# Performance work log

Measured on AMD Instinct MI355X. Metric: run time of the kernel, lower is better.

The kernel has to match this reference:

```python
import jax, jax.numpy as jnp
import numpy as np

B, IN_DIM, HID, DIM, M = 4096, 256, 200, 512, 256


def setup_inputs() -> dict:
    key = jax.random.key(0)
    ks = jax.random.split(key, 9)
    x = jax.random.normal(ks[0], (B, IN_DIM), dtype=jnp.float32)
    # per-sample polytope RHS; strictly positive so y=0 is always feasible
    b = jax.random.uniform(ks[1], (B, M), dtype=jnp.float32) + 1.0
    W1 = jax.random.normal(ks[2], (IN_DIM, HID), dtype=jnp.float32) / np.sqrt(IN_DIM)
    b1 = jnp.zeros((HID,), dtype=jnp.float32)
    W2 = jax.random.normal(ks[3], (HID, HID), dtype=jnp.float32) / np.sqrt(HID)
    b2 = jnp.zeros((HID,), dtype=jnp.float32)
    W3 = jax.random.normal(ks[4], (HID, DIM), dtype=jnp.float32) / np.sqrt(HID)
    b3 = jnp.zeros((DIM,), dtype=jnp.float32)
    # constraint matrix A: polytope {y : A y <= b}
    A = jax.random.normal(ks[5], (M, DIM), dtype=jnp.float32) / np.sqrt(DIM)
    return {"x": x, "b": b, "W1": W1, "b1": b1, "W2": W2, "b2": b2,
            "W3": W3, "b3": b3, "A": A, "step": 0, "n_iter": 100}


def _mlp(x, W1, b1, W2, b2, W3, b3):
    h = jax.nn.relu(x @ W1 + b1)
    h = jax.nn.relu(h @ W2 + b2)
    return h @ W3 + b3  # [B, DIM]


def _project(y0, b, A, n_iter):
    """Euclidean projection of y0 onto {y : A y <= b} via dual projected gradient.
    y(lam) = y0 - A^T lam;  lam <- relu(lam + t (A y(lam) - b))."""
    t = 1.0 / jnp.sum(A * A)  # 1/||A||_F^2 <= 1/sigma_max(A)^2 -> convergent step

    def body(lam, _):
        y = y0 - lam @ A                      # [B, DIM]
        lam = jax.nn.relu(lam + t * (y @ A.T - b))  # [B, M]
        return lam, None

    lam0 = jnp.zeros_like(b)
    lam, _ = jax.lax.scan(body, lam0, None, length=n_iter)
    return y0 - lam @ A


def reference(x, b, W1, b1, W2, b2, W3, b3, A, step, n_iter):
    y0 = _mlp(x, W1, b1, W2, b2, W3, b3)
    # optax.linear_schedule(0.0, 0.0, 2000, 300) is identically zero
    alpha = jnp.float32(0.0)
    y = _project(y0, b, A, n_iter)
    return (1.0 - alpha) * y + alpha * y0
```

## Files before the change

kernel.cpp:

```cpp
#include <hip/hip_runtime.h>
#include <hip/hip_bf16.h>
#include <stdint.h>


typedef __attribute__((ext_vector_type(8))) short bf16x8;
typedef __attribute__((ext_vector_type(4))) float f32x4;
typedef __attribute__((ext_vector_type(4))) unsigned short u16x4;

__device__ __forceinline__ unsigned short f2b(float f) {
  union { float f; uint32_t u; } v; v.f = f;
  uint32_t r = (v.u + 0x7FFFu + ((v.u >> 16) & 1u)) >> 16;
  return (unsigned short)r;
}
__device__ __forceinline__ float b2f(unsigned short h) {
  union { uint32_t u; float f; } v; v.u = ((uint32_t)h) << 16;
  return v.f;
}
__device__ __forceinline__ unsigned int pk2(float a, float b) {
  __hip_bfloat162 h = __float22bfloat162_rn(make_float2(a, b));
  unsigned int u; __builtin_memcpy(&u, &h, 4); return u;
}
__device__ __forceinline__ float ldf(const void* p, int idx, int f32f) {
  return f32f ? ((const float*)p)[idx] : b2f(((const unsigned short*)p)[idx]);
}
__device__ __forceinline__ f32x4 mfma16(bf16x8 a, bf16x8 b, f32x4 c) {
  return __builtin_amdgcn_mfma_f32_16x16x32_bf16(a, b, c, 0, 0, 0);
}
__device__ __forceinline__ bf16x8 ld8(const void* p, int idx, int f32f) {
  bf16x8 r;
  if (f32f) {
    float4 a0 = *(const float4*)((const float*)p + idx);
    float4 a1 = *(const float4*)((const float*)p + idx + 4);
    r[0]=(short)f2b(a0.x); r[1]=(short)f2b(a0.y); r[2]=(short)f2b(a0.z); r[3]=(short)f2b(a0.w);
    r[4]=(short)f2b(a1.x); r[5]=(short)f2b(a1.y); r[6]=(short)f2b(a1.z); r[7]=(short)f2b(a1.w);
  } else {
    r = *(const bf16x8*)((const unsigned short*)p + idx);
  }
  return r;
}
__device__ __forceinline__ int sniff(const void* p) {
  unsigned short h = ((const unsigned short*)p)[threadIdx.x & 63];
  unsigned e = (h >> 7) & 0xFFu;
  return (__ballot(e >= 132u) != 0ull) ? 1 : 0;
}

__device__ __forceinline__ void swiz_one(const void* __restrict__ src,
                                         unsigned short* __restrict__ dst, int e,
                                         int Ksrc, int Nsrc, int ld, bool trans,
                                         int NCT, int f32f) {
  const int j = e & 7, lane = (e >> 3) & 63, rest = e >> 9;
  const int nt = rest % NCT, kk = rest / NCT;
  const int k = kk * 32 + ((lane >> 4) << 3) + j;
  const int n = nt * 16 + (lane & 15);
  unsigned short v = 0;
  if (k < Ksrc && n < Nsrc)
    v = f2b(ldf(src, trans ? n * ld + k : k * ld + n, f32f));
  dst[e] = v;
}

__global__ __launch_bounds__(256) void prep_kernel(
    const void* __restrict__ W1, const void* __restrict__ W2,
    const void* __restrict__ W3, const void* __restrict__ Am,
    unsigned short* __restrict__ Gsw, float* __restrict__ slot,
    unsigned short* __restrict__ W1sw, unsigned short* __restrict__ W2sw,
    unsigned short* __restrict__ W3sw, unsigned short* __restrict__ ATsw,
    unsigned short* __restrict__ Asw) {
  const int f32f = sniff(Am);
  const int tid = threadIdx.x;
  if (blockIdx.x < 256) {
    if (tid >= 64) return;
    const int lane = tid, r16 = lane & 15, q = lane >> 4;
    const int ti = blockIdx.x >> 4, tj = blockIdx.x & 15;
    const int rowA = (16 * ti + r16) * 512;
    const int rowB = (16 * tj + r16) * 512;
    f32x4 acc = {0.f, 0.f, 0.f, 0.f};
    #pragma unroll
    for (int kk = 0; kk < 16; ++kk) {
      const int col = 32 * kk + 8 * q;
      bf16x8 afr = ld8(Am, rowA + col, f32f);
      bf16x8 bfr = ld8(Am, rowB + col, f32f);
      acc = mfma16(afr, bfr, acc);
    }
    #pragma unroll
    for (int rg = 0; rg < 4; ++rg) {
      const int mrow = 16 * ti + 4 * q + rg;
      const int kk2 = mrow >> 5, q2 = (mrow >> 3) & 3, j = mrow & 7;
      Gsw[((kk2 * 16 + tj) * 64 + (q2 * 16 + r16)) * 8 + j] = f2b(acc[rg]);
    }
    if (ti == tj) {
      float d = ((r16 >> 2) == q) ? acc[r16 & 3] : 0.0f;
      #pragma unroll
      for (int off = 32; off >= 1; off >>= 1) d += __shfl_xor(d, off, 64);
      if (lane == 0) slot[ti] = d;
    }
    return;
  }
  int idx = (blockIdx.x - 256) * 256 + tid;
  if (idx < 53248)  { swiz_one(W1, W1sw, idx, 256, 200, 200, false, 13, f32f); return; }
  idx -= 53248;
  if (idx < 46592)  { swiz_one(W2, W2sw, idx, 200, 200, 200, false, 13, f32f); return; }
  idx -= 46592;
  if (idx < 114688) { swiz_one(W3, W3sw, idx, 200, 512, 512, false, 32, f32f); return; }
  idx -= 114688;
  if (idx < 131072) { swiz_one(Am, ATsw, idx, 512, 256, 512, true, 16, f32f); return; }
  idx -= 131072;
  swiz_one(Am, Asw, idx, 256, 512, 512, false, 32, f32f);
}

__global__ __launch_bounds__(512, 2) void mega_kernel(
    const void* __restrict__ x,
    const void* __restrict__ bmat,
    const void* __restrict__ b1,
    const void* __restrict__ b2,
    const void* __restrict__ b3,
    const float* __restrict__ slot,
    const unsigned short* __restrict__ Gsw,
    const unsigned short* __restrict__ W1sw,
    const unsigned short* __restrict__ W2sw,
    const unsigned short* __restrict__ W3sw,
    const unsigned short* __restrict__ ATsw,
    const unsigned short* __restrict__ Asw,
    float* __restrict__ out)
{
  __shared__ __attribute__((aligned(16))) unsigned short xbuf[16 * 264];
  __shared__ __attribute__((aligned(16))) unsigned short hbuf[16 * 232];
  __shared__ __attribute__((aligned(16))) unsigned short ybuf[16 * 520];
  __shared__ __attribute__((aligned(16))) unsigned short lbuf[2][16 * 264];
  __shared__ __attribute__((aligned(16))) float yf32[16 * 516];

  const int tid = threadIdx.x;
  const int lane = tid & 63;
  const int w = tid >> 6;
  const int r16 = lane & 15;
  const int q = lane >> 4;
  const int rowbase = blockIdx.x << 4;
  const int f32f = sniff(x);

  {
    const int rr = tid >> 5;
    const int c8 = (tid & 31) << 3;
    if (f32f) {
      const float4* sp = (const float4*)((const float*)x + (rowbase + rr) * 256 + c8);
      float4 v0 = sp[0], v1 = sp[1];
      u16x4 p0 = {f2b(v0.x), f2b(v0.y), f2b(v0.z), f2b(v0.w)};
      u16x4 p1 = {f2b(v1.x), f2b(v1.y), f2b(v1.z), f2b(v1.w)};
      *(u16x4*)&xbuf[rr * 264 + c8]     = p0;
      *(u16x4*)&xbuf[rr * 264 + c8 + 4] = p1;
    } else {
      *(bf16x8*)&xbuf[rr * 264 + c8] =
          *(const bf16x8*)((const unsigned short*)x + (rowbase + rr) * 256 + c8);
    }
    if (tid < 256) hbuf[(tid >> 4) * 232 + 208 + (tid & 15)] = 0;
  }
  __syncthreads();
  float tr = 0.0f;
  #pragma unroll
  for (int i = 0; i < 16; ++i) tr += slot[i];
  const float t = 1.0f / tr;

  f32x4 a1[2];
  #pragma unroll
  for (int i = 0; i < 2; ++i) a1[i] = (f32x4){0.f, 0.f, 0.f, 0.f};
  #pragma unroll
  for (int kk = 0; kk < 8; ++kk) {
    bf16x8 bx = *(const bf16x8*)&xbuf[r16 * 264 + 32 * kk + 8 * q];
    #pragma unroll
    for (int i = 0; i < 2; ++i) {
      const int nt = w + 8 * i;
      if (nt < 13) {
        bf16x8 af = *(const bf16x8*)(W1sw + ((kk * 13 + nt) * 64 + lane) * 8);
        a1[i] = mfma16(af, bx, a1[i]);
      }
    }
  }
  #pragma unroll
  for (int i = 0; i < 2; ++i) {
    const int nt = w + 8 * i;
    if (nt < 13) {
      u16x4 pk;
      #pragma unroll
      for (int rg = 0; rg < 4; ++rg) {
        const int n = 16 * nt + 4 * q + rg;
        const float bias = (n < 200) ? ldf(b1, n, f32f) : 0.0f;
        pk[rg] = f2b(fmaxf(a1[i][rg] + bias, 0.0f));
      }
      *(u16x4*)&hbuf[r16 * 232 + 16 * nt + 4 * q] = pk;
    }
  }
  __syncthreads();

  f32x4 a2[2];
  #pragma unroll
  for (int i = 0; i < 2; ++i) a2[i] = (f32x4){0.f, 0.f, 0.f, 0.f};
  #pragma unroll
  for (int kk = 0; kk < 7; ++kk) {
    bf16x8 bh = *(const bf16x8*)&hbuf[r16 * 232 + 32 * kk + 8 * q];
    #pragma unroll
    for (int i = 0; i < 2; ++i) {
      const int nt = w + 8 * i;
      if (nt < 13) {
        bf16x8 af = *(const bf16x8*)(W2sw + ((kk * 13 + nt) * 64 + lane) * 8);
        a2[i] = mfma16(af, bh, a2[i]);
      }
    }
  }
  __syncthreads();
  #pragma unroll
  for (int i = 0; i < 2; ++i) {
    const int nt = w + 8 * i;
    if (nt < 13) {
      u16x4 pk;
      #pragma unroll
      for (int rg = 0; rg < 4; ++rg) {
        const int n = 16 * nt + 4 * q + rg;
        const float bias = (n < 200) ? ldf(b2, n, f32f) : 0.0f;
        pk[rg] = f2b(fmaxf(a2[i][rg] + bias, 0.0f));
      }
      *(u16x4*)&hbuf[r16 * 232 + 16 * nt + 4 * q] = pk;
    }
  }
  __syncthreads();

  {
    f32x4 y0a[4];
    #pragma unroll
    for (int i = 0; i < 4; ++i) y0a[i] = (f32x4){0.f, 0.f, 0.f, 0.f};
    #pragma unroll
    for (int kk = 0; kk < 7; ++kk) {
      bf16x8 bh = *(const bf16x8*)&hbuf[r16 * 232 + 32 * kk + 8 * q];
      #pragma unroll
      for (int i = 0; i < 4; ++i) {
        const int nt = 4 * w + i;
        bf16x8 af = *(const bf16x8*)(W3sw + ((kk * 32 + nt) * 64 + lane) * 8);
        y0a[i] = mfma16(af, bh, y0a[i]);
      }
    }
    #pragma unroll
    for (int i = 0; i < 4; ++i) {
      const int nt = 4 * w + i;
      u16x4 pk;
      #pragma unroll
      for (int rg = 0; rg < 4; ++rg) {
        y0a[i][rg] += ldf(b3, 16 * nt + 4 * q + rg, f32f);
        pk[rg] = f2b(y0a[i][rg]);
      }
      *(u16x4*)&ybuf[r16 * 520 + 16 * nt + 4 * q] = pk;
      float4 sf = {y0a[i][0], y0a[i][1], y0a[i][2], y0a[i][3]};
      *(float4*)&yf32[r16 * 516 + 16 * nt + 4 * q] = sf;
    }
  }
  __syncthreads();

  f32x4 tc[4], base[4];
  if (w < 4) {
    f32x4 cacc[4];
    #pragma unroll
    for (int i = 0; i < 4; ++i) {
      const int mt = w + 4 * i;
      if (f32f) {
        float4 bb = *(const float4*)((const float*)bmat + (rowbase + r16) * 256 + 16 * mt + 4 * q);
        cacc[i] = (f32x4){-bb.x, -bb.y, -bb.z, -bb.w};
      } else {
        u16x4 bb = *(const u16x4*)((const unsigned short*)bmat + (rowbase + r16) * 256 + 16 * mt + 4 * q);
        #pragma unroll
        for (int rg = 0; rg < 4; ++rg) cacc[i][rg] = -b2f(bb[rg]);
      }
    }
    #pragma unroll
    for (int kk = 0; kk < 16; ++kk) {
      bf16x8 by = *(const bf16x8*)&ybuf[r16 * 520 + 32 * kk + 8 * q];
      #pragma unroll
      for (int i = 0; i < 4; ++i) {
        bf16x8 af = *(const bf16x8*)(ATsw + ((kk * 16 + w + 4 * i) * 64 + lane) * 8);
        cacc[i] = mfma16(af, by, cacc[i]);
      }
    }
    #pragma unroll
    for (int i = 0; i < 4; ++i) {
      #pragma unroll
      for (int rg = 0; rg < 4; ++rg) {
        tc[i][rg] = t * cacc[i][rg];
        base[i][rg] = fmaxf(tc[i][rg], 0.0f) + tc[i][rg];
      }
      const unsigned int lo = pk2(fmaxf(tc[i][0], 0.f), fmaxf(tc[i][1], 0.f));
      const unsigned int hi = pk2(fmaxf(tc[i][2], 0.f), fmaxf(tc[i][3], 0.f));
      *(uint2*)&lbuf[0][r16 * 264 + 16 * (w + 4 * i) + 4 * q] = make_uint2(lo, hi);
    }
  }

  bf16x8 gA0, gA1, gA2, gA3, gA4, gA5, gA6, gA7;
  bf16x8 gB0, gB1, gB2, gB3, gB4, gB5, gB6, gB7;
  bf16x8 gC0, gC1, gC2, gC3, gC4, gC5, gC6, gC7;
  bf16x8 gD0, gD1, gD2, gD3, gD4, gD5, gD6, gD7;
  if (w < 4) {
    #define GLD(j, i) (*(const bf16x8*)(Gsw + (((j) * 16 + w + 4 * (i)) * 64 + lane) * 8))
    gA0 = GLD(0,0); gA1 = GLD(1,0); gA2 = GLD(2,0); gA3 = GLD(3,0);
    gA4 = GLD(4,0); gA5 = GLD(5,0); gA6 = GLD(6,0); gA7 = GLD(7,0);
    gB0 = GLD(0,1); gB1 = GLD(1,1); gB2 = GLD(2,1); gB3 = GLD(3,1);
    gB4 = GLD(4,1); gB5 = GLD(5,1); gB6 = GLD(6,1); gB7 = GLD(7,1);
    gC0 = GLD(0,2); gC1 = GLD(1,2); gC2 = GLD(2,2); gC3 = GLD(3,2);
    gC4 = GLD(4,2); gC5 = GLD(5,2); gC6 = GLD(6,2); gC7 = GLD(7,2);
    gD0 = GLD(0,3); gD1 = GLD(1,3); gD2 = GLD(2,3); gD3 = GLD(3,3);
    gD4 = GLD(4,3); gD5 = GLD(5,3); gD6 = GLD(6,3); gD7 = GLD(7,3);
    #undef GLD
    asm volatile("" : "+v"(gA0), "+v"(gA1), "+v"(gA2), "+v"(gA3),
                      "+v"(gA4), "+v"(gA5), "+v"(gA6), "+v"(gA7),
                      "+v"(gB0), "+v"(gB1), "+v"(gB2), "+v"(gB3),
                      "+v"(gB4), "+v"(gB5), "+v"(gB6), "+v"(gB7));
    asm volatile("" : "+v"(gC0), "+v"(gC1), "+v"(gC2), "+v"(gC3),
                      "+v"(gC4), "+v"(gC5), "+v"(gC6), "+v"(gC7),
                      "+v"(gD0), "+v"(gD1), "+v"(gD2), "+v"(gD3),
                      "+v"(gD4), "+v"(gD5), "+v"(gD6), "+v"(gD7));
  }
  __syncthreads();

  #define PGD_J(j, blv) \
    acc0 = mfma16(gA##j, blv, acc0); acc1 = mfma16(gB##j, blv, acc1); \
    acc2 = mfma16(gC##j, blv, acc2); acc3 = mfma16(gD##j, blv, acc3);
  int cur = 0;
  for (int it = 0; it < 99; ++it) {
    if (w < 4) {
      const unsigned short* lb = &lbuf[cur][r16 * 264 + 8 * q];
      const bf16x8 bl0 = *(const bf16x8*)(lb);
      const bf16x8 bl1 = *(const bf16x8*)(lb + 32);
      const bf16x8 bl2 = *(const bf16x8*)(lb + 64);
      const bf16x8 bl3 = *(const bf16x8*)(lb + 96);
      const bf16x8 bl4 = *(const bf16x8*)(lb + 128);
      const bf16x8 bl5 = *(const bf16x8*)(lb + 160);
      const bf16x8 bl6 = *(const bf16x8*)(lb + 192);
      const bf16x8 bl7 = *(const bf16x8*)(lb + 224);
      f32x4 acc0 = {0.f, 0.f, 0.f, 0.f}, acc1 = {0.f, 0.f, 0.f, 0.f};
      f32x4 acc2 = {0.f, 0.f, 0.f, 0.f}, acc3 = {0.f, 0.f, 0.f, 0.f};
      PGD_J(0, bl0)  PGD_J(1, bl1)  PGD_J(2, bl2)  PGD_J(3, bl3)
      PGD_J(4, bl4)  PGD_J(5, bl5)  PGD_J(6, bl6)  PGD_J(7, bl7)
      const unsigned int sx = (it == 98) ? 0x80008000u : 0u;
      const int nxt = cur ^ 1;
      {
        f32x4 v;
        #pragma unroll
        for (int rg = 0; rg < 4; ++rg)
          v[rg] = fmaxf(fmaf(-t, acc0[rg], base[0][rg]), 0.0f);
        *(uint2*)&lbuf[nxt][r16 * 264 + 16 * w + 4 * q] =
            make_uint2(pk2(v[0], v[1]) ^ sx, pk2(v[2], v[3]) ^ sx);
        #pragma unroll
        for (int rg = 0; rg < 4; ++rg) base[0][rg] = v[rg] + tc[0][rg];
      }
      {
        f32x4 v;
        #pragma unroll
        for (int rg = 0; rg < 4; ++rg)
          v[rg] = fmaxf(fmaf(-t, acc1[rg], base[1][rg]), 0.0f);
        *(uint2*)&lbuf[nxt][r16 * 264 + 16 * (w + 4) + 4 * q] =
            make_uint2(pk2(v[0], v[1]) ^ sx, pk2(v[2], v[3]) ^ sx);
        #pragma unroll
        for (int rg = 0; rg < 4; ++rg) base[1][rg] = v[rg] + tc[1][rg];
      }
      {
        f32x4 v;
        #pragma unroll
        for (int rg = 0; rg < 4; ++rg)
          v[rg] = fmaxf(fmaf(-t, acc2[rg], base[2][rg]), 0.0f);
        *(uint2*)&lbuf[nxt][r16 * 264 + 16 * (w + 8) + 4 * q] =
            make_uint2(pk2(v[0], v[1]) ^ sx, pk2(v[2], v[3]) ^ sx);
        #pragma unroll
        for (int rg = 0; rg < 4; ++rg) base[2][rg] = v[rg] + tc[2][rg];
      }
      {
        f32x4 v;
        #pragma unroll
        for (int rg = 0; rg < 4; ++rg)
          v[rg] = fmaxf(fmaf(-t, acc3[rg], base[3][rg]), 0.0f);
        *(uint2*)&lbuf[nxt][r16 * 264 + 16 * (w + 12) + 4 * q] =
            make_uint2(pk2(v[0], v[1]) ^ sx, pk2(v[2], v[3]) ^ sx);
        #pragma unroll
        for (int rg = 0; rg < 4; ++rg) base[3][rg] = v[rg] + tc[3][rg];
      }
    }
    __syncthreads();
    cur ^= 1;
  }
  #undef PGD_J

  f32x4 yo[4];
  #pragma unroll
  for (int i = 0; i < 4; ++i) {
    float4 v = *(const float4*)&yf32[r16 * 516 + 16 * (4 * w + i) + 4 * q];
    yo[i] = (f32x4){v.x, v.y, v.z, v.w};
  }
  #pragma unroll
  for (int kk = 0; kk < 8; ++kk) {
    bf16x8 bl = *(const bf16x8*)&lbuf[cur][r16 * 264 + 32 * kk + 8 * q];
    #pragma unroll
    for (int i = 0; i < 4; ++i) {
      bf16x8 af = *(const bf16x8*)(Asw + ((kk * 32 + 4 * w + i) * 64 + lane) * 8);
      yo[i] = mfma16(af, bl, yo[i]);
    }
  }
  #pragma unroll
  for (int i = 0; i < 4; ++i) {
    const int nt = 4 * w + i;
    float4 st = {yo[i][0], yo[i][1], yo[i][2], yo[i][3]};
    *(float4*)(out + (size_t)(rowbase + r16) * 512 + 16 * nt + 4 * q) = st;
  }
}

extern "C" void kernel_launch(void* const* d_in, const int* in_sizes, int n_in,
                              void* d_out, int out_size, void* d_ws, size_t ws_size,
                              hipStream_t stream) {
  const void* x  = d_in[0];
  const void* bm = d_in[1];
  const void* W1 = d_in[2];
  const void* b1 = d_in[3];
  const void* W2 = d_in[4];
  const void* b2 = d_in[5];
  const void* W3 = d_in[6];
  const void* b3 = d_in[7];
  const void* Am = d_in[8];

  float* slot = (float*)d_ws;
  unsigned short* Gsw  = (unsigned short*)d_ws + 128;
  unsigned short* W1sw = Gsw  + 65536;
  unsigned short* W2sw = W1sw + 53248;
  unsigned short* W3sw = W2sw + 46592;
  unsigned short* ATsw = W3sw + 114688;
  unsigned short* Asw  = ATsw + 131072;

  prep_kernel<<<2118, 256, 0, stream>>>(W1, W2, W3, Am, Gsw, slot,
                                        W1sw, W2sw, W3sw, ATsw, Asw);
  mega_kernel<<<256, 512, 0, stream>>>(x, bm, b1, b2, b3, slot,
                                       Gsw, W1sw, W2sw, W3sw, ATsw, Asw,
                                       (float*)d_out);
}
```

Measured before the change: 89.30 us.

## Spread dual-gradient loop across all eight waves with half-row tiles

The projection iteration previously ran only on waves 0-3, each computing a full 16-row MFMA tile. Now all eight waves take part: each wave pair handles 8 rows, with rows duplicated inside the 16-row MFMA tile, and only the first 8 lanes-rows write results. The aim is to use the idle waves to hide MFMA and LDS latency in the serial 99-iteration loop. In exchange, half of every MFMA output is wasted, total MFMA issue per SIMD doubles, and all waves now hold the G fragments in registers.

```diff
diff --git a/kernel.cpp b/kernel.cpp
--- a/kernel.cpp
+++ b/kernel.cpp
@@ -251,135 +251,113 @@
   }
   __syncthreads();
 
-  f32x4 tc[4], base[4];
-  if (w < 4) {
+  const int tm = w >> 2;
+  const int wv = w & 3;
+  const int rrd = 8 * tm + (r16 & 7);
+  const int wrow = (8 * tm + r16) * 264 + 4 * q;
+
+  f32x4 tc0, tc1, tc2, tc3, ba0, ba1, ba2, ba3;
+  {
     f32x4 cacc[4];
     #pragma unroll
     for (int i = 0; i < 4; ++i) {
-      const int mt = w + 4 * i;
+      const int mt = wv + 4 * i;
       if (f32f) {
-        float4 bb = *(const float4*)((const float*)bmat + (rowbase + r16) * 256 + 16 * mt + 4 * q);
+        float4 bb = *(const float4*)((const float*)bmat + (rowbase + rrd) * 256 + 16 * mt + 4 * q);
         cacc[i] = (f32x4){-bb.x, -bb.y, -bb.z, -bb.w};
       } else {
-        u16x4 bb = *(const u16x4*)((const unsigned short*)bmat + (rowbase + r16) * 256 + 16 * mt + 4 * q);
+        u16x4 bb = *(const u16x4*)((const unsigned short*)bmat + (rowbase + rrd) * 256 + 16 * mt + 4 * q);
         #pragma unroll
         for (int rg = 0; rg < 4; ++rg) cacc[i][rg] = -b2f(bb[rg]);
       }
     }
     #pragma unroll
     for (int kk = 0; kk < 16; ++kk) {
-      bf16x8 by = *(const bf16x8*)&ybuf[r16 * 520 + 32 * kk + 8 * q];
+      bf16x8 by = *(const bf16x8*)&ybuf[rrd * 520 + 32 * kk + 8 * q];
       #pragma unroll
       for (int i = 0; i < 4; ++i) {
-        bf16x8 af = *(const bf16x8*)(ATsw + ((kk * 16 + w + 4 * i) * 64 + lane) * 8);
+        bf16x8 af = *(const bf16x8*)(ATsw + ((kk * 16 + wv + 4 * i) * 64 + lane) * 8);
         cacc[i] = mfma16(af, by, cacc[i]);
       }
     }
+    f32x4 tcl[4], bal[4];
     #pragma unroll
     for (int i = 0; i < 4; ++i) {
       #pragma unroll
       for (int rg = 0; rg < 4; ++rg) {
-        tc[i][rg] = t * cacc[i][rg];
-        base[i][rg] = fmaxf(tc[i][rg], 0.0f) + tc[i][rg];
-      }
-      const unsigned int lo = pk2(fmaxf(tc[i][0], 0.f), fmaxf(tc[i][1], 0.f));
-      const unsigned int hi = pk2(fmaxf(tc[i][2], 0.f), fmaxf(tc[i][3], 0.f));
-      *(uint2*)&lbuf[0][r16 * 264 + 16 * (w + 4 * i) + 4 * q] = make_uint2(lo, hi);
-    }
-  }
-
-  bf16x8 gA0, gA1, gA2, gA3, gA4, gA5, gA6, gA7;
-  bf16x8 gB0, gB1, gB2, gB3, gB4, gB5, gB6, gB7;
-  bf16x8 gC0, gC1, gC2, gC3, gC4, gC5, gC6, gC7;
-  bf16x8 gD0, gD1, gD2, gD3, gD4, gD5, gD6, gD7;
-  if (w < 4) {
-    #define GLD(j, i) (*(const bf16x8*)(Gsw + (((j) * 16 + w + 4 * (i)) * 64 + lane) * 8))
-    gA0 = GLD(0,0); gA1 = GLD(1,0); gA2 = GLD(2,0); gA3 = GLD(3,0);
-    gA4 = GLD(4,0); gA5 = GLD(5,0); gA6 = GLD(6,0); gA7 = GLD(7,0);
-    gB0 = GLD(0,1); gB1 = GLD(1,1); gB2 = GLD(2,1); gB3 = GLD(3,1);
-    gB4 = GLD(4,1); gB5 = GLD(5,1); gB6 = GLD(6,1); gB7 = GLD(7,1);
-    gC0 = GLD(0,2); gC1 = GLD(1,2); gC2 = GLD(2,2); gC3 = GLD(3,2);
-    gC4 = GLD(4,2); gC5 = GLD(5,2); gC6 = GLD(6,2); gC7 = GLD(7,2);
-    gD0 = GLD(0,3); gD1 = GLD(1,3); gD2 = GLD(2,3); gD3 = GLD(3,3);
-    gD4 = GLD(4,3); gD5 = GLD(5,3); gD6 = GLD(6,3); gD7 = GLD(7,3);
-    #undef GLD
-    asm volatile("" : "+v"(gA0), "+v"(gA1), "+v"(gA2), "+v"(gA3),
-                      "+v"(gA4), "+v"(gA5), "+v"(gA6), "+v"(gA7),
-                      "+v"(gB0), "+v"(gB1), "+v"(gB2), "+v"(gB3),
-                      "+v"(gB4), "+v"(gB5), "+v"(gB6), "+v"(gB7));
-    asm volatile("" : "+v"(gC0), "+v"(gC1), "+v"(gC2), "+v"(gC3),
-                      "+v"(gC4), "+v"(gC5), "+v"(gC6), "+v"(gC7),
-                      "+v"(gD0), "+v"(gD1), "+v"(gD2), "+v"(gD3),
-                      "+v"(gD4), "+v"(gD5), "+v"(gD6), "+v"(gD7));
-  }
+        tcl[i][rg] = t * cacc[i][rg];
+        bal[i][rg] = fmaxf(tcl[i][rg], 0.0f) + tcl[i][rg];
+      }
+      if (r16 < 8) {
+        const unsigned int lo = pk2(fmaxf(tcl[i][0], 0.f), fmaxf(tcl[i][1], 0.f));
+        const unsigned int hi = pk2(fmaxf(tcl[i][2], 0.f), fmaxf(tcl[i][3], 0.f));
+        *(uint2*)&lbuf[0][wrow + 16 * (wv + 4 * i)] = make_uint2(lo, hi);
+      }
+    }
+    tc0 = tcl[0]; tc1 = tcl[1]; tc2 = tcl[2]; tc3 = tcl[3];
+    ba0 = bal[0]; ba1 = bal[1]; ba2 = bal[2]; ba3 = bal[3];
+  }
+
+  #define GLD(j, i) (*(const bf16x8*)(Gsw + (((j) * 16 + wv + 4 * (i)) * 64 + lane) * 8))
+  bf16x8 gA0 = GLD(0,0), gA1 = GLD(1,0), gA2 = GLD(2,0), gA3 = GLD(3,0);
+  bf16x8 gA4 = GLD(4,0), gA5 = GLD(5,0), gA6 = GLD(6,0), gA7 = GLD(7,0);
+  bf16x8 gB0 = GLD(0,1), gB1 = GLD(1,1), gB2 = GLD(2,1), gB3 = GLD(3,1);
+  bf16x8 gB4 = GLD(4,1), gB5 = GLD(5,1), gB6 = GLD(6,1), gB7 = GLD(7,1);
+  bf16x8 gC0 = GLD(0,2), gC1 = GLD(1,2), gC2 = GLD(2,2), gC3 = GLD(3,2);
+  bf16x8 gC4 = GLD(4,2), gC5 = GLD(5,2), gC6 = GLD(6,2), gC7 = GLD(7,2);
+  bf16x8 gD0 = GLD(0,3), gD1 = GLD(1,3), gD2 = GLD(2,3), gD3 = GLD(3,3);
+  bf16x8 gD4 = GLD(4,3), gD5 = GLD(5,3), gD6 = GLD(6,3), gD7 = GLD(7,3);
+  #undef GLD
+  asm volatile("" : "+v"(gA0), "+v"(gA1), "+v"(gA2), "+v"(gA3),
+                    "+v"(gA4), "+v"(gA5), "+v"(gA6), "+v"(gA7),
+                    "+v"(gB0), "+v"(gB1), "+v"(gB2), "+v"(gB3),
+                    "+v"(gB4), "+v"(gB5), "+v"(gB6), "+v"(gB7));
+  asm volatile("" : "+v"(gC0), "+v"(gC1), "+v"(gC2), "+v"(gC3),
+                    "+v"(gC4), "+v"(gC5), "+v"(gC6), "+v"(gC7),
+                    "+v"(gD0), "+v"(gD1), "+v"(gD2), "+v"(gD3),
+                    "+v"(gD4), "+v"(gD5), "+v"(gD6), "+v"(gD7));
+  const int cbase = rrd * 264 + 8 * q;
   __syncthreads();
 
   #define PGD_J(j, blv) \
     acc0 = mfma16(gA##j, blv, acc0); acc1 = mfma16(gB##j, blv, acc1); \
     acc2 = mfma16(gC##j, blv, acc2); acc3 = mfma16(gD##j, blv, acc3);
+  #define PGD_EPI(i, accv, tcv, bav) {                                        \
+    f32x4 vv;                                                                 \
+    _Pragma("unroll")                                                         \
+    for (int rg = 0; rg < 4; ++rg)                                            \
+      vv[rg] = fmaxf(fmaf(-t, accv[rg], bav[rg]), 0.0f);                      \
+    if (r16 < 8)                                                              \
+      *(uint2*)&lbuf[nxt][wrow + 16 * (wv + 4 * (i))] =                       \
+          make_uint2(pk2(vv[0], vv[1]) ^ sx, pk2(vv[2], vv[3]) ^ sx);         \
+    _Pragma("unroll")                                                         \
+    for (int rg = 0; rg < 4; ++rg) bav[rg] = vv[rg] + tcv[rg]; }
   int cur = 0;
   for (int it = 0; it < 99; ++it) {
-    if (w < 4) {
-      const unsigned short* lb = &lbuf[cur][r16 * 264 + 8 * q];
-      const bf16x8 bl0 = *(const bf16x8*)(lb);
-      const bf16x8 bl1 = *(const bf16x8*)(lb + 32);
-      const bf16x8 bl2 = *(const bf16x8*)(lb + 64);
-      const bf16x8 bl3 = *(const bf16x8*)(lb + 96);
-      const bf16x8 bl4 = *(const bf16x8*)(lb + 128);
-      const bf16x8 bl5 = *(const bf16x8*)(lb + 160);
-      const bf16x8 bl6 = *(const bf16x8*)(lb + 192);
-      const bf16x8 bl7 = *(const bf16x8*)(lb + 224);
-      f32x4 acc0 = {0.f, 0.f, 0.f, 0.f}, acc1 = {0.f, 0.f, 0.f, 0.f};
-      f32x4 acc2 = {0.f, 0.f, 0.f, 0.f}, acc3 = {0.f, 0.f, 0.f, 0.f};
-      PGD_J(0, bl0)  PGD_J(1, bl1)  PGD_J(2, bl2)  PGD_J(3, bl3)
-      PGD_J(4, bl4)  PGD_J(5, bl5)  PGD_J(6, bl6)  PGD_J(7, bl7)
-      const unsigned int sx = (it == 98) ? 0x80008000u : 0u;
-      const int nxt = cur ^ 1;
-      {
-        f32x4 v;
-        #pragma unroll
-        for (int rg = 0; rg < 4; ++rg)
-          v[rg] = fmaxf(fmaf(-t, acc0[rg], base[0][rg]), 0.0f);
-        *(uint2*)&lbuf[nxt][r16 * 264 + 16 * w + 4 * q] =
-            make_uint2(pk2(v[0], v[1]) ^ sx, pk2(v[2], v[3]) ^ sx);
-        #pragma unroll
-        for (int rg = 0; rg < 4; ++rg) base[0][rg] = v[rg] + tc[0][rg];
-      }
-      {
-        f32x4 v;
-        #pragma unroll
-        for (int rg = 0; rg < 4; ++rg)
-          v[rg] = fmaxf(fmaf(-t, acc1[rg], base[1][rg]), 0.0f);
-        *(uint2*)&lbuf[nxt][r16 * 264 + 16 * (w + 4) + 4 * q] =
-            make_uint2(pk2(v[0], v[1]) ^ sx, pk2(v[2], v[3]) ^ sx);
-        #pragma unroll
-        for (int rg = 0; rg < 4; ++rg) base[1][rg] = v[rg] + tc[1][rg];
-      }
-      {
-        f32x4 v;
-        #pragma unroll
-        for (int rg = 0; rg < 4; ++rg)
-          v[rg] = fmaxf(fmaf(-t, acc2[rg], base[2][rg]), 0.0f);
-        *(uint2*)&lbuf[nxt][r16 * 264 + 16 * (w + 8) + 4 * q] =
-            make_uint2(pk2(v[0], v[1]) ^ sx, pk2(v[2], v[3]) ^ sx);
-        #pragma unroll
-        for (int rg = 0; rg < 4; ++rg) base[2][rg] = v[rg] + tc[2][rg];
-      }
-      {
-        f32x4 v;
-        #pragma unroll
-        for (int rg = 0; rg < 4; ++rg)
-          v[rg] = fmaxf(fmaf(-t, acc3[rg], base[3][rg]), 0.0f);
-        *(uint2*)&lbuf[nxt][r16 * 264 + 16 * (w + 12) + 4 * q] =
-            make_uint2(pk2(v[0], v[1]) ^ sx, pk2(v[2], v[3]) ^ sx);
-        #pragma unroll
-        for (int rg = 0; rg < 4; ++rg) base[3][rg] = v[rg] + tc[3][rg];
-      }
-    }
+    const unsigned short* lb = lbuf[cur] + cbase;
+    const bf16x8 bl0 = *(const bf16x8*)(lb);
+    const bf16x8 bl1 = *(const bf16x8*)(lb + 32);
+    const bf16x8 bl2 = *(const bf16x8*)(lb + 64);
+    const bf16x8 bl3 = *(const bf16x8*)(lb + 96);
+    const bf16x8 bl4 = *(const bf16x8*)(lb + 128);
+    const bf16x8 bl5 = *(const bf16x8*)(lb + 160);
+    const bf16x8 bl6 = *(const bf16x8*)(lb + 192);
+    const bf16x8 bl7 = *(const bf16x8*)(lb + 224);
+    f32x4 acc0 = {0.f,0.f,0.f,0.f}, acc1 = {0.f,0.f,0.f,0.f};
+    f32x4 acc2 = {0.f,0.f,0.f,0.f}, acc3 = {0.f,0.f,0.f,0.f};
+    PGD_J(0, bl0)  PGD_J(1, bl1)  PGD_J(2, bl2)  PGD_J(3, bl3)
+    PGD_J(4, bl4)  PGD_J(5, bl5)  PGD_J(6, bl6)  PGD_J(7, bl7)
+    const unsigned int sx = (it == 98) ? 0x80008000u : 0u;
+    const int nxt = cur ^ 1;
+    PGD_EPI(0, acc0, tc0, ba0)
+    PGD_EPI(1, acc1, tc1, ba1)
+    PGD_EPI(2, acc2, tc2, ba2)
+    PGD_EPI(3, acc3, tc3, ba3)
     __syncthreads();
-    cur ^= 1;
+    cur = nxt;
   }
   #undef PGD_J
+  #undef PGD_EPI
 
   f32x4 yo[4];
   #pragma unroll
```

New measurement: 120.7 us. 35.2% more time.
